# Kernel optimization log

Measured on AMD Instinct MI355X. Metric: run time of the kernel, lower is better.

## Reference

```python
import jax, jax.numpy as jnp
import numpy as np

B, N, E = 64, 2048, 32768          # graphs, nodes/graph, edges/graph
DIM = 64
RATIO = 0.8
K1 = int(np.ceil(RATIO * N))        # 1639 nodes/graph after pool1
K2 = int(np.ceil(RATIO * K1))       # 1312 nodes/graph after pool2
NUM_CLASSES = 6


def gcn_conv(x, W, b, src, dst, valid, n):
    # GCNConv with self-loops: out = D^-1/2 (A+I) D^-1/2 (x W) + b
    xw = x @ W                                          # [n, DIM]
    deg = jnp.zeros(n, x.dtype).at[dst].add(valid) + 1.0  # in-degree incl. self-loop
    norm = valid * jax.lax.rsqrt(deg[src] * deg[dst])      # per-edge norm (0 for masked)
    agg = jnp.zeros_like(xw).at[dst].add(xw[src] * norm[:, None])
    return agg + xw / deg[:, None] + b                  # self-loop term has norm 1/deg


def topk_pool(x, p, n_graphs, n_per, k):
    # PyG TopKPooling: score = tanh(x.p/||p||); keep top-k per graph; gate x by score
    score = jnp.tanh((x @ p) / jnp.linalg.norm(p))       # [n_graphs*n_per]
    vals, idx = jax.lax.top_k(score.reshape(n_graphs, n_per), k)  # [n_graphs, k]
    xg = x.reshape(n_graphs, n_per, -1)
    sel = jnp.take_along_axis(xg, idx[..., None], axis=1)          # [n_graphs, k, DIM]
    xp = sel * vals[..., None]
    perm = (idx + (jnp.arange(n_graphs) * n_per)[:, None]).reshape(-1)  # global ids kept
    return xp.reshape(n_graphs * k, -1), perm


def global_max_mean(x, n_graphs, n_per):
    xg = x.reshape(n_graphs, n_per, -1)
    return jnp.concatenate([xg.max(axis=1), xg.mean(axis=1)], axis=1)  # [n_graphs, 2*DIM]


def forward(x, edge_index, batch, W1, b1, p1, W2, b2, p2, lin1_w, lin1_b, lin2_w, lin2_b):
    src, dst = edge_index[0], edge_index[1]
    n_total = B * N
    ones = jnp.ones(src.shape[0], x.dtype)

    x = jax.nn.relu(gcn_conv(x, W1, b1, src, dst, ones, n_total))
    x, perm = topk_pool(x, p1, B, N, K1)
    x1 = global_max_mean(x, B, K1)

    # filter_adj: reindex edges to surviving nodes; drop (mask) edges touching removed nodes
    new_id = jnp.full(n_total, -1, jnp.int32).at[perm].set(jnp.arange(B * K1, dtype=jnp.int32))
    s2, d2 = new_id[src], new_id[dst]
    valid = ((s2 >= 0) & (d2 >= 0)).astype(x.dtype)
    s2 = jnp.where(s2 >= 0, s2, 0)
    d2 = jnp.where(d2 >= 0, d2, 0)

    x = jax.nn.relu(gcn_conv(x, W2, b2, s2, d2, valid, B * K1))
    x, _ = topk_pool(x, p2, B, K1, K2)
    x2 = global_max_mean(x, B, K2)

    h = x1 + x2
    h = jax.nn.relu(h @ lin1_w + lin1_b)
    return h @ lin2_w + lin2_b                           # [B, NUM_CLASSES]


def setup_inputs():
    key = jax.random.key(0)
    ks = jax.random.split(key, 10)
    x = jax.random.normal(ks[0], (B * N, DIM), jnp.float32)
    off = (jnp.arange(B) * N)[:, None]
    src = (jax.random.randint(ks[1], (B, E), 0, N) + off).reshape(-1)
    dst = (jax.random.randint(ks[2], (B, E), 0, N) + off).reshape(-1)
    edge_index = jnp.stack([src, dst]).astype(jnp.int32)
    batch = jnp.repeat(jnp.arange(B, dtype=jnp.int32), N)
    s = 1.0 / np.sqrt(DIM)
    return {
        "x": x,
        "edge_index": edge_index,
        "batch": batch,
        "W1": jax.random.normal(ks[3], (DIM, DIM), jnp.float32) * s,
        "b1": jnp.zeros(DIM, jnp.float32),
        "p1": jax.random.normal(ks[4], (DIM,), jnp.float32) * s,
        "W2": jax.random.normal(ks[5], (DIM, DIM), jnp.float32) * s,
        "b2": jnp.zeros(DIM, jnp.float32),
        "p2": jax.random.normal(ks[6], (DIM,), jnp.float32) * s,
        "lin1_w": jax.random.normal(ks[7], (2 * DIM, DIM), jnp.float32) / np.sqrt(2 * DIM),
        "lin1_b": jnp.zeros(DIM, jnp.float32),
        "lin2_w": jax.random.normal(ks[8], (DIM, NUM_CLASSES), jnp.float32) * s,
        "lin2_b": jnp.zeros(NUM_CLASSES, jnp.float32),
    }


def reference(x, edge_index, batch, W1, b1, p1, W2, b2, p2, lin1_w, lin1_b, lin2_w, lin2_b):
    return forward(x, edge_index, batch, W1, b1, p1, W2, b2, p2, lin1_w, lin1_b, lin2_w, lin2_b)
```

## Files before the change

### kernel.cpp

```cpp
#include <hip/hip_runtime.h>
#include <hip/hip_bf16.h>
#include <cstdint>
#include <cstddef>

#define B_    64
#define N_    2048
#define E_    32768
#define DIM_  64
#define K1_   1639
#define K2_   1312
#define NTOT  (B_ * N_)
#define ETOT  (B_ * E_)
#define N2TOT (B_ * K1_)
#define NCLS  6
#define PB_   8
#define CHUNKS_ 16
#define SLICES_ 16
#define BCAP  3072
#define REG_  192

typedef short bf8 __attribute__((ext_vector_type(8)));
typedef float f4  __attribute__((ext_vector_type(4)));

static __device__ __forceinline__ float2 bf2f(unsigned u) {
    float2 r;
    r.x = __uint_as_float(u << 16);
    r.y = __uint_as_float(u & 0xFFFF0000u);
    return r;
}
static __device__ __forceinline__ unsigned f2bf(float a, float b) {
    __hip_bfloat162 h = __float22bfloat162_rn(make_float2(a, b));
    unsigned u;
    __builtin_memcpy(&u, &h, 4);
    return u;
}
static __device__ __forceinline__ unsigned short f2bf_rn(float v) {
    unsigned u = __float_as_uint(v);
    return (unsigned short)((u + 0x7FFFu + ((u >> 16) & 1u)) >> 16);
}

template<int STAGE>
__launch_bounds__(256)
__global__ void k_bucket(const int* src, const int* dst, const int* remap,
                         int* bcnt, unsigned int* blist) {
    const int LSTR = (STAGE == 1) ? 128 : 103;
    __shared__ unsigned int lb[CHUNKS_][REG_];
    __shared__ int lc[CHUNKS_];
    int b = blockIdx.x;
    int g = b & 63, slice = b >> 6;
    int tid = threadIdx.x;
    if (tid < CHUNKS_) lc[tid] = 0;
    __syncthreads();
    const int ESL = E_ / SLICES_;
    const int* sp = src + (size_t)g * E_ + slice * ESL;
    const int* dp = dst + (size_t)g * E_ + slice * ESL;
    int gbase = g * ((STAGE == 1) ? N_ : K1_);
    for (int e = tid * 4; e < ESL; e += 1024) {
        int4 ss = *(const int4*)&sp[e];
        int4 dd = *(const int4*)&dp[e];
#pragma unroll
        for (int t = 0; t < 4; t++) {
            int s = (&ss.x)[t], d = (&dd.x)[t];
            if (STAGE == 2) {
                s = remap[s]; d = remap[d];
                if ((s | d) < 0) continue;
                s -= gbase; d -= gbase;
            } else {
                s &= (N_ - 1); d &= (N_ - 1);
            }
            int ch = d / LSTR;
            int dl = d - ch * LSTR;
            int p = atomicAdd(&lc[ch], 1);
            if (p < REG_) lb[ch][p] = ((unsigned)dl << 12) | (unsigned)s;
        }
    }
    __syncthreads();
    for (int ch = 0; ch < CHUNKS_; ch++) {
        int n = min(lc[ch], REG_);
        unsigned int* out = blist + (size_t)(g * CHUNKS_ + ch) * BCAP + slice * REG_;
        for (int i = tid; i < n; i += 256) out[i] = lb[ch][i];
    }
    if (tid < CHUNKS_) bcnt[(g * SLICES_ + slice) * CHUNKS_ + tid] = min(lc[tid], REG_);
}

template<int STAGE>
__launch_bounds__(256)
__global__ void k_sort(const int* bcnt, unsigned int* blist,
                       const float* xsrc, const int* sel, const float* vals,
                       unsigned int* xb, int* ninfo) {
    const int NL   = (STAGE == 1) ? N_ : K1_;
    const int LSTR = (STAGE == 1) ? 128 : 103;
    __shared__ int cnt[128], st[128], cur[128], cnt_s[SLICES_];
    __shared__ float rsqv[128];
    __shared__ unsigned short sorted[BCAP];
    int b = blockIdx.x;
    int g = b & 63, ch = b >> 6;
    int tid = threadIdx.x;
    if (tid < 128) { cnt[tid] = 0; cur[tid] = 0; }
    if (tid < SLICES_) cnt_s[tid] = bcnt[(g * SLICES_ + tid) * CHUNKS_ + ch];
    __syncthreads();
    size_t bb = (size_t)(g * CHUNKS_ + ch) * BCAP;
    const unsigned int* bl = blist + bb;
    for (int s = 0; s < SLICES_; s++) {
        int ns = cnt_s[s];
        for (int i = tid; i < ns; i += 256) atomicAdd(&cnt[bl[s * REG_ + i] >> 12], 1);
    }
    __syncthreads();
    if (tid < 128) st[tid] = cnt[tid];
    __syncthreads();
    for (int o = 1; o < 128; o <<= 1) {
        int add = (tid >= o && tid < 128) ? st[tid - o] : 0;
        __syncthreads();
        if (tid < 128) st[tid] += add;
        __syncthreads();
    }
    for (int s = 0; s < SLICES_; s++) {
        int ns = cnt_s[s];
        for (int i = tid; i < ns; i += 256) {
            unsigned pk = bl[s * REG_ + i];
            int dl = (int)(pk >> 12);
            int p = st[dl] - cnt[dl] + atomicAdd(&cur[dl], 1);
            sorted[p] = (unsigned short)(pk & 0xFFFu);
        }
    }
    __syncthreads();
    int n = st[127];
    for (int i = tid; i < n; i += 256) blist[bb + i] = (unsigned int)sorted[i];
    int lo = ch * LSTR;
    int nloc = min(LSTR, NL - lo);
    int gbase = g * NL;
    if (tid < nloc) {
        int node = gbase + lo + tid;
        int c = cnt[tid];
        int start = (int)bb + st[tid] - c;
        ninfo[node] = (start << 8) | min(c, 255);
        rsqv[tid] = rsqrtf((float)(c + 1));
    }
    __syncthreads();
    const float2* xs = (const float2*)xsrc;
    for (int idx = tid; idx < nloc * 32; idx += 256) {
        int nl = idx >> 5, f2 = idx & 31;
        int node = gbase + lo + nl;
        int rowp; float sc;
        if (STAGE == 2) { rowp = sel[node]; sc = vals[node] * rsqv[nl]; }
        else            { rowp = node;      sc = rsqv[nl]; }
        float2 v = xs[(size_t)rowp * 32 + f2];
        xb[(size_t)node * 32 + f2] = f2bf(v.x * sc, v.y * sc);
    }
}

template<bool GATE>
__launch_bounds__(256)
__global__ void k_agg(const unsigned int* xb, const int* ninfo, const unsigned int* csr,
                      float* y) {
    int b = blockIdx.x;
    int xcd = b & 7, r = b >> 3;
    int graph, local;
    if (GATE) {
        graph = xcd * 8 + r / 410;
        local = (r % 410) * 4 + (threadIdx.x >> 6);
        if (local >= K1_) return;
    } else {
        graph = xcd * 8 + (r >> 9);
        local = (r & 511) * 4 + (threadIdx.x >> 6);
    }
    const int NL = GATE ? K1_ : N_;
    int node = graph * NL + local;
    int lane = threadIdx.x & 63;
    int half = lane >> 5;
    int fpos = lane & 31;
    int ni = ninfo[node];
    int cnt = ni & 255, base = ni >> 8;
    float rd = rsqrtf((float)(cnt + 1));
    float ax = 0.f, ay = 0.f, bx = 0.f, by = 0.f;
    float cx = 0.f, cy = 0.f, dx = 0.f, dy = 0.f;
    int gbase = graph * NL;
    for (int chunk = 0; chunk < cnt; chunk += 64) {
        int nch = min(64, cnt - chunk);
        int sv = 0;
        if (lane < nch) sv = gbase + (int)csr[base + chunk + lane];
        int i = 0;
        for (; i + 8 <= nch; i += 8) {
            int s0 = __shfl(sv, i + half),     s1 = __shfl(sv, i + 2 + half),
                s2 = __shfl(sv, i + 4 + half), s3 = __shfl(sv, i + 6 + half);
            unsigned u0 = xb[(size_t)s0 * 32 + fpos];
            unsigned u1 = xb[(size_t)s1 * 32 + fpos];
            unsigned u2 = xb[(size_t)s2 * 32 + fpos];
            unsigned u3 = xb[(size_t)s3 * 32 + fpos];
            float2 f0 = bf2f(u0), f1 = bf2f(u1), f2 = bf2f(u2), f3 = bf2f(u3);
            ax += f0.x; ay += f0.y;
            bx += f1.x; by += f1.y;
            cx += f2.x; cy += f2.y;
            dx += f3.x; dy += f3.y;
        }
        for (; i + 4 <= nch; i += 4) {
            int s0 = __shfl(sv, i + half), s1 = __shfl(sv, i + 2 + half);
            unsigned u0 = xb[(size_t)s0 * 32 + fpos];
            unsigned u1 = xb[(size_t)s1 * 32 + fpos];
            float2 f0 = bf2f(u0), f1 = bf2f(u1);
            ax += f0.x; ay += f0.y;
            bx += f1.x; by += f1.y;
        }
        for (; i < nch; i += 2) {
            int idx = i + half;
            int s0 = __shfl(sv, idx & 63);
            float m = (idx < nch) ? 1.f : 0.f;
            float2 f0 = bf2f(xb[(size_t)s0 * 32 + fpos]);
            ax += f0.x * m; ay += f0.y * m;
        }
    }
    float sx = (ax + bx) + (cx + dx), sy = (ay + by) + (cy + dy);
    sx += __shfl(sx, lane ^ 32);
    sy += __shfl(sy, lane ^ 32);
    if (half == 0) {
        float2 fs = bf2f(xb[(size_t)node * 32 + fpos]);
        float2 o;
        o.x = (sx + fs.x) * rd;
        o.y = (sy + fs.y) * rd;
        ((float2*)y)[(size_t)node * 32 + fpos] = o;
    }
}

__launch_bounds__(256)
__global__ void k_convrow(float* y, const float* W, const float* bias, const float* pvec,
                          float* score, int rows) {
    int wid  = threadIdx.x >> 6;
    int lane = threadIdx.x & 63;
    int rowbase = blockIdx.x * 64 + wid * 16;
    int q = lane >> 4, c = lane & 15;
    bf8 bh[2][4], blo[2][4];
#pragma unroll
    for (int ks = 0; ks < 2; ks++)
#pragma unroll
        for (int nt = 0; nt < 4; nt++) {
            bf8 h, l;
#pragma unroll
            for (int j = 0; j < 8; j++) {
                float wv = W[(ks * 32 + q * 8 + j) * 64 + nt * 16 + c];
                unsigned short hb = f2bf_rn(wv);
                h[j] = (short)hb;
                l[j] = (short)f2bf_rn(wv - __uint_as_float((unsigned)hb << 16));
            }
            bh[ks][nt] = h; blo[ks][nt] = l;
        }
    const float* yr = y + (size_t)(rowbase + c) * DIM_ + q * 8;
    bf8 ah[2], al[2];
#pragma unroll
    for (int ks = 0; ks < 2; ks++) {
        float4 v0 = *(const float4*)(yr + ks * 32);
        float4 v1 = *(const float4*)(yr + ks * 32 + 4);
        float vv[8] = {v0.x, v0.y, v0.z, v0.w, v1.x, v1.y, v1.z, v1.w};
        bf8 h, l;
#pragma unroll
        for (int j = 0; j < 8; j++) {
            unsigned short hb = f2bf_rn(vv[j]);
            h[j] = (short)hb;
            l[j] = (short)f2bf_rn(vv[j] - __uint_as_float((unsigned)hb << 16));
        }
        ah[ks] = h; al[ks] = l;
    }
    float pp = 0.f;
#pragma unroll
    for (int i = 0; i < DIM_; i++) pp += pvec[i] * pvec[i];
    float rpn = rsqrtf(pp);
    float dot[4] = {0.f, 0.f, 0.f, 0.f};
#pragma unroll
    for (int nt = 0; nt < 4; nt++) {
        f4 acc = {0.f, 0.f, 0.f, 0.f};
#pragma unroll
        for (int ks = 0; ks < 2; ks++) {
            acc = __builtin_amdgcn_mfma_f32_16x16x32_bf16(ah[ks], bh[ks][nt],  acc, 0, 0, 0);
            acc = __builtin_amdgcn_mfma_f32_16x16x32_bf16(ah[ks], blo[ks][nt], acc, 0, 0, 0);
            acc = __builtin_amdgcn_mfma_f32_16x16x32_bf16(al[ks], bh[ks][nt],  acc, 0, 0, 0);
        }
        float bcol = bias[nt * 16 + c];
        float pcol = pvec[nt * 16 + c];
        float st[4];
#pragma unroll
        for (int reg = 0; reg < 4; reg++) {
            float v = fmaxf(acc[reg] + bcol, 0.f);
            st[reg] = v;
            dot[reg] += v * pcol;
        }
#pragma unroll
        for (int reg = 0; reg < 4; reg++)
            y[(size_t)(rowbase + q * 4 + reg) * DIM_ + nt * 16 + c] = st[reg];
    }
#pragma unroll
    for (int m = 1; m < 16; m <<= 1) {
#pragma unroll
        for (int reg = 0; reg < 4; reg++) dot[reg] += __shfl_xor(dot[reg], m);
    }
    if (c == 0) {
#pragma unroll
        for (int reg = 0; reg < 4; reg++)
            score[rowbase + q * 4 + reg] = tanhf(dot[reg] * rpn);
    }
    (void)rows;
}

template<int STAGE>
__launch_bounds__(256)
__global__ void k_select(const float* score, int* new_id, int* sel, float* vals) {
    const int Nin = (STAGE == 1) ? N_ : K1_;
    const int K   = (STAGE == 1) ? K1_ : K2_;
    __shared__ unsigned long long keys[N_];
    __shared__ int bins[256], ts[256];
    __shared__ unsigned long long s_prefix;
    __shared__ int s_need, s_cnt;
    int g = blockIdx.x, tid = threadIdx.x;
    const float* sg = score + (size_t)g * Nin;
    for (int i = tid; i < Nin; i += 256) {
        unsigned u = __float_as_uint(sg[i]);
        u = (u & 0x80000000u) ? ~u : (u | 0x80000000u);
        keys[i] = ((unsigned long long)u << 11) | (unsigned long long)(2047 - i);
    }
    if (tid == 0) { s_need = K; s_prefix = 0ull; s_cnt = 0; }
    __syncthreads();
    for (int shift = 40; shift >= 0; shift -= 8) {
        bins[tid] = 0;
        __syncthreads();
        unsigned long long pref = s_prefix;
        int need = s_need;
        int hi = shift + 8;
        for (int i = tid; i < Nin; i += 256) {
            unsigned long long k = keys[i];
            if ((k >> hi) == pref) atomicAdd(&bins[(int)((k >> shift) & 255)], 1);
        }
        __syncthreads();
        ts[tid] = bins[tid];
        __syncthreads();
        for (int o = 1; o < 256; o <<= 1) {
            int add = (tid + o < 256) ? ts[tid + o] : 0;
            __syncthreads();
            ts[tid] += add;
            __syncthreads();
        }
        int nxt = (tid == 255) ? 0 : ts[tid + 1];
        if (ts[tid] >= need && nxt < need) {
            s_prefix = (pref << 8) | (unsigned long long)tid;
            s_need = need - nxt;
        }
        __syncthreads();
    }
    unsigned long long T = s_prefix;
    for (int i = tid; i < Nin; i += 256) {
        if (keys[i] >= T) {
            int r = atomicAdd(&s_cnt, 1);
            int slot = g * K + r;
            sel[slot]  = g * Nin + i;
            vals[slot] = sg[i];
            if (STAGE == 1) new_id[g * N_ + i] = slot;
        } else if (STAGE == 1) {
            new_id[g * N_ + i] = -1;
        }
    }
}

template<int STAGE>
__launch_bounds__(256)
__global__ void k_pool(const float* conv, const int* sel, const float* vals, float* part) {
    const int K = (STAGE == 1) ? K1_ : K2_;
    int b = blockIdx.x;
    int g = b & 63, c = b >> 6;
    int wv = threadIdx.x >> 6, lane = threadIdx.x & 63;
    float mx = -3.402823466e38f, sm = 0.f;
    for (int r = c * 4 + wv; r < K; r += PB_ * 4) {
        int slot = g * K + r;
        int row  = sel[slot];
        float val = vals[slot];
        float v = conv[(size_t)row * DIM_ + lane] * val;
        mx = fmaxf(mx, v);
        sm += v;
    }
    __shared__ float rmx[4][64], rsm[4][64];
    rmx[wv][lane] = mx; rsm[wv][lane] = sm;
    __syncthreads();
    if (wv == 0) {
        mx = fmaxf(fmaxf(rmx[0][lane], rmx[1][lane]), fmaxf(rmx[2][lane], rmx[3][lane]));
        sm = rsm[0][lane] + rsm[1][lane] + rsm[2][lane] + rsm[3][lane];
        part[((size_t)(g * PB_ + c) * 2 + 0) * 64 + lane] = mx;
        part[((size_t)(g * PB_ + c) * 2 + 1) * 64 + lane] = sm;
    }
}

__launch_bounds__(64)
__global__ void k_head(const float* part1, const float* part2,
                       const float* l1w, const float* l1b,
                       const float* l2w, const float* l2b, float* out) {
    __shared__ float h[128];
    __shared__ float h1[64];
    int g = blockIdx.x, t = threadIdx.x;
    float mx1 = -3.402823466e38f, sm1 = 0.f, mx2 = -3.402823466e38f, sm2 = 0.f;
#pragma unroll
    for (int c = 0; c < PB_; c++) {
        mx1 = fmaxf(mx1, part1[((size_t)(g * PB_ + c) * 2 + 0) * 64 + t]);
        sm1 += part1[((size_t)(g * PB_ + c) * 2 + 1) * 64 + t];
        mx2 = fmaxf(mx2, part2[((size_t)(g * PB_ + c) * 2 + 0) * 64 + t]);
        sm2 += part2[((size_t)(g * PB_ + c) * 2 + 1) * 64 + t];
    }
    h[t]      = mx1 + mx2;
    h[t + 64] = sm1 / (float)K1_ + sm2 / (float)K2_;
    __syncthreads();
    float acc = l1b[t];
#pragma unroll 8
    for (int i = 0; i < 128; i++) acc += h[i] * l1w[i * 64 + t];
    h1[t] = fmaxf(acc, 0.0f);
    __syncthreads();
    if (t < NCLS) {
        float o = l2b[t];
#pragma unroll
        for (int i = 0; i < 64; i++) o += h1[i] * l2w[i * NCLS + t];
        out[g * NCLS + t] = o;
    }
}

extern "C" void kernel_launch(void* const* d_in, const int* in_sizes, int n_in,
                              void* d_out, int out_size, void* d_ws, size_t ws_size,
                              hipStream_t stream) {
    const float* x   = (const float*)d_in[0];
    const int*   ei  = (const int*)d_in[1];
    const int*   src = ei;
    const int*   dst = ei + ETOT;
    const float* W1  = (const float*)d_in[3];
    const float* b1  = (const float*)d_in[4];
    const float* p1  = (const float*)d_in[5];
    const float* W2  = (const float*)d_in[6];
    const float* b2  = (const float*)d_in[7];
    const float* p2  = (const float*)d_in[8];
    const float* l1w = (const float*)d_in[9];
    const float* l1b = (const float*)d_in[10];
    const float* l2w = (const float*)d_in[11];
    const float* l2b = (const float*)d_in[12];
    (void)in_sizes; (void)n_in; (void)out_size; (void)ws_size;

    char* ws = (char*)d_ws;
    size_t off = 0;
    auto alloc = [&](size_t bytes) -> void* {
        void* p = ws + off;
        off = (off + bytes + 255) & ~(size_t)255;
        return p;
    };
    float*        bufA  = (float*)       alloc((size_t)NTOT  * DIM_ * 4);
    float*        bufB  = (float*)       alloc((size_t)N2TOT * DIM_ * 4);
    unsigned int* blist = (unsigned int*)alloc((size_t)B_ * CHUNKS_ * BCAP * 4);
    unsigned int* xb    = (unsigned int*)alloc((size_t)NTOT * 32 * 4);
    int*          bcnt  = (int*)         alloc((size_t)B_ * SLICES_ * CHUNKS_ * 4);
    int*          ninfo = (int*)         alloc((size_t)NTOT * 4);
    float*        score = (float*)       alloc((size_t)NTOT * 4);
    int*          newid = (int*)         alloc((size_t)NTOT * 4);
    int*          sel1  = (int*)         alloc((size_t)N2TOT * 4);
    float*        vals1 = (float*)       alloc((size_t)N2TOT * 4);
    int*          sel2  = (int*)         alloc((size_t)B_ * K2_ * 4);
    float*        vals2 = (float*)       alloc((size_t)B_ * K2_ * 4);
    float*        part1 = (float*)       alloc((size_t)B_ * PB_ * 128 * 4);
    float*        part2 = (float*)       alloc((size_t)B_ * PB_ * 128 * 4);

    k_bucket<1><<<B_ * SLICES_, 256, 0, stream>>>(src, dst, nullptr, bcnt, blist);
    k_sort<1><<<B_ * CHUNKS_, 256, 0, stream>>>(bcnt, blist, x, nullptr, nullptr, xb, ninfo);
    k_agg<false><<<NTOT / 4, 256, 0, stream>>>(xb, ninfo, blist, bufA);
    k_convrow<<<NTOT / 64, 256, 0, stream>>>(bufA, W1, b1, p1, score, NTOT);
    k_select<1><<<B_, 256, 0, stream>>>(score, newid, sel1, vals1);
    k_pool<1><<<B_ * PB_, 256, 0, stream>>>(bufA, sel1, vals1, part1);

    k_bucket<2><<<B_ * SLICES_, 256, 0, stream>>>(src, dst, newid, bcnt, blist);
    k_sort<2><<<B_ * CHUNKS_, 256, 0, stream>>>(bcnt, blist, bufA, sel1, vals1, xb, ninfo);
    k_agg<true><<<410 * B_, 256, 0, stream>>>(xb, ninfo, blist, bufB);
    k_convrow<<<N2TOT / 64, 256, 0, stream>>>(bufB, W2, b2, p2, score, N2TOT);
    k_select<2><<<B_, 256, 0, stream>>>(score, nullptr, sel2, vals2);
    k_pool<2><<<B_ * PB_, 256, 0, stream>>>(bufB, sel2, vals2, part2);

    k_head<<<B_, 64, 0, stream>>>(part1, part2, l1w, l1b, l2w, l2b, (float*)d_out);
}
```

Baseline: 355.2 us.

## Stage remap in LDS, prescale CSR indices, wave-level scans, emit pooled bf16 features

Several independent tweaks. k_bucket stage 2 stages the per-graph remap table in shared memory instead of reading it from global memory for every edge. k_sort flattens its slice loops, replaces the block-wide Hillis-Steele scan with wave shuffle scans, and stores neighbour indices pre-multiplied by 32. k_agg uses those scaled indices to skip a multiply. k_select gets a shuffle-based suffix scan with fewer barriers. k_pool stage 1 also writes the gated pooled rows as bf16 into a compact buffer (aliased onto bufB), so stage-2 sort reads contiguous bf16 instead of gathering fp32 rows via sel and vals; this adds an extra bf16 rounding step.

```diff
diff --git a/kernel.cpp b/kernel.cpp
--- a/kernel.cpp
+++ b/kernel.cpp
@@ -46,10 +46,13 @@
     const int LSTR = (STAGE == 1) ? 128 : 103;
     __shared__ unsigned int lb[CHUNKS_][REG_];
     __shared__ int lc[CHUNKS_];
+    __shared__ int rm[N_];
     int b = blockIdx.x;
     int g = b & 63, slice = b >> 6;
     int tid = threadIdx.x;
     if (tid < CHUNKS_) lc[tid] = 0;
+    if (STAGE == 2)
+        for (int i = tid; i < N_; i += 256) rm[i] = remap[g * N_ + i];
     __syncthreads();
     const int ESL = E_ / SLICES_;
     const int* sp = src + (size_t)g * E_ + slice * ESL;
@@ -62,7 +65,7 @@
         for (int t = 0; t < 4; t++) {
             int s = (&ss.x)[t], d = (&dd.x)[t];
             if (STAGE == 2) {
-                s = remap[s]; d = remap[d];
+                s = rm[s & (N_ - 1)]; d = rm[d & (N_ - 1)];
                 if ((s | d) < 0) continue;
                 s -= gbase; d -= gbase;
             } else {
@@ -86,11 +89,11 @@
 template<int STAGE>
 __launch_bounds__(256)
 __global__ void k_sort(const int* bcnt, unsigned int* blist,
-                       const float* xsrc, const int* sel, const float* vals,
+                       const float* xf, const unsigned int* xg,
                        unsigned int* xb, int* ninfo) {
     const int NL   = (STAGE == 1) ? N_ : K1_;
     const int LSTR = (STAGE == 1) ? 128 : 103;
-    __shared__ int cnt[128], st[128], cur[128], cnt_s[SLICES_];
+    __shared__ int cnt[128], st[128], cur[128], cnt_s[SLICES_], stot[2];
     __shared__ float rsqv[128];
     __shared__ unsigned short sorted[BCAP];
     int b = blockIdx.x;
@@ -101,23 +104,30 @@
     __syncthreads();
     size_t bb = (size_t)(g * CHUNKS_ + ch) * BCAP;
     const unsigned int* bl = blist + bb;
-    for (int s = 0; s < SLICES_; s++) {
-        int ns = cnt_s[s];
-        for (int i = tid; i < ns; i += 256) atomicAdd(&cnt[bl[s * REG_ + i] >> 12], 1);
-    }
-    __syncthreads();
-    if (tid < 128) st[tid] = cnt[tid];
-    __syncthreads();
-    for (int o = 1; o < 128; o <<= 1) {
-        int add = (tid >= o && tid < 128) ? st[tid - o] : 0;
-        __syncthreads();
-        if (tid < 128) st[tid] += add;
-        __syncthreads();
-    }
-    for (int s = 0; s < SLICES_; s++) {
-        int ns = cnt_s[s];
-        for (int i = tid; i < ns; i += 256) {
-            unsigned pk = bl[s * REG_ + i];
+    const int TOT = SLICES_ * REG_;
+    for (int i = tid; i < TOT; i += 256) {
+        int s = i / REG_, j = i - s * REG_;
+        if (j < cnt_s[s]) atomicAdd(&cnt[bl[i] >> 12], 1);
+    }
+    __syncthreads();
+    if (tid < 128) {
+        int v = cnt[tid];
+        int l64 = tid & 63;
+#pragma unroll
+        for (int o = 1; o < 64; o <<= 1) {
+            int t = __shfl_up(v, o);
+            if (l64 >= o) v += t;
+        }
+        st[tid] = v;
+        if (l64 == 63) stot[tid >> 6] = v;
+    }
+    __syncthreads();
+    if (tid >= 64 && tid < 128) st[tid] += stot[0];
+    __syncthreads();
+    for (int i = tid; i < TOT; i += 256) {
+        int s = i / REG_, j = i - s * REG_;
+        if (j < cnt_s[s]) {
+            unsigned pk = bl[i];
             int dl = (int)(pk >> 12);
             int p = st[dl] - cnt[dl] + atomicAdd(&cur[dl], 1);
             sorted[p] = (unsigned short)(pk & 0xFFFu);
@@ -125,7 +135,7 @@
     }
     __syncthreads();
     int n = st[127];
-    for (int i = tid; i < n; i += 256) blist[bb + i] = (unsigned int)sorted[i];
+    for (int i = tid; i < n; i += 256) blist[bb + i] = ((unsigned int)sorted[i]) << 5;
     int lo = ch * LSTR;
     int nloc = min(LSTR, NL - lo);
     int gbase = g * NL;
@@ -137,14 +147,13 @@
         rsqv[tid] = rsqrtf((float)(c + 1));
     }
     __syncthreads();
-    const float2* xs = (const float2*)xsrc;
     for (int idx = tid; idx < nloc * 32; idx += 256) {
         int nl = idx >> 5, f2 = idx & 31;
         int node = gbase + lo + nl;
-        int rowp; float sc;
-        if (STAGE == 2) { rowp = sel[node]; sc = vals[node] * rsqv[nl]; }
-        else            { rowp = node;      sc = rsqv[nl]; }
-        float2 v = xs[(size_t)rowp * 32 + f2];
+        float sc = rsqv[nl];
+        float2 v;
+        if (STAGE == 1) v = ((const float2*)xf)[(size_t)node * 32 + f2];
+        else            v = bf2f(xg[(size_t)node * 32 + f2]);
         xb[(size_t)node * 32 + f2] = f2bf(v.x * sc, v.y * sc);
     }
 }
@@ -174,19 +183,19 @@
     float rd = rsqrtf((float)(cnt + 1));
     float ax = 0.f, ay = 0.f, bx = 0.f, by = 0.f;
     float cx = 0.f, cy = 0.f, dx = 0.f, dy = 0.f;
-    int gbase = graph * NL;
+    int gbase32 = graph * NL * 32;
     for (int chunk = 0; chunk < cnt; chunk += 64) {
         int nch = min(64, cnt - chunk);
         int sv = 0;
-        if (lane < nch) sv = gbase + (int)csr[base + chunk + lane];
+        if (lane < nch) sv = gbase32 + (int)csr[base + chunk + lane];
         int i = 0;
         for (; i + 8 <= nch; i += 8) {
             int s0 = __shfl(sv, i + half),     s1 = __shfl(sv, i + 2 + half),
                 s2 = __shfl(sv, i + 4 + half), s3 = __shfl(sv, i + 6 + half);
-            unsigned u0 = xb[(size_t)s0 * 32 + fpos];
-            unsigned u1 = xb[(size_t)s1 * 32 + fpos];
-            unsigned u2 = xb[(size_t)s2 * 32 + fpos];
-            unsigned u3 = xb[(size_t)s3 * 32 + fpos];
+            unsigned u0 = xb[(size_t)(s0 + fpos)];
+            unsigned u1 = xb[(size_t)(s1 + fpos)];
+            unsigned u2 = xb[(size_t)(s2 + fpos)];
+            unsigned u3 = xb[(size_t)(s3 + fpos)];
             float2 f0 = bf2f(u0), f1 = bf2f(u1), f2 = bf2f(u2), f3 = bf2f(u3);
             ax += f0.x; ay += f0.y;
             bx += f1.x; by += f1.y;
@@ -195,9 +204,8 @@
         }
         for (; i + 4 <= nch; i += 4) {
             int s0 = __shfl(sv, i + half), s1 = __shfl(sv, i + 2 + half);
-            unsigned u0 = xb[(size_t)s0 * 32 + fpos];
-            unsigned u1 = xb[(size_t)s1 * 32 + fpos];
-            float2 f0 = bf2f(u0), f1 = bf2f(u1);
+            float2 f0 = bf2f(xb[(size_t)(s0 + fpos)]);
+            float2 f1 = bf2f(xb[(size_t)(s1 + fpos)]);
             ax += f0.x; ay += f0.y;
             bx += f1.x; by += f1.y;
         }
@@ -205,7 +213,7 @@
             int idx = i + half;
             int s0 = __shfl(sv, idx & 63);
             float m = (idx < nch) ? 1.f : 0.f;
-            float2 f0 = bf2f(xb[(size_t)s0 * 32 + fpos]);
+            float2 f0 = bf2f(xb[(size_t)(s0 + fpos)]);
             ax += f0.x * m; ay += f0.y * m;
         }
     }
@@ -305,10 +313,11 @@
     const int Nin = (STAGE == 1) ? N_ : K1_;
     const int K   = (STAGE == 1) ? K1_ : K2_;
     __shared__ unsigned long long keys[N_];
-    __shared__ int bins[256], ts[256];
+    __shared__ int bins[256], wsum[4];
     __shared__ unsigned long long s_prefix;
     __shared__ int s_need, s_cnt;
     int g = blockIdx.x, tid = threadIdx.x;
+    int l64 = tid & 63, wid = tid >> 6;
     const float* sg = score + (size_t)g * Nin;
     for (int i = tid; i < Nin; i += 256) {
         unsigned u = __float_as_uint(sg[i]);
@@ -328,16 +337,18 @@
             if ((k >> hi) == pref) atomicAdd(&bins[(int)((k >> shift) & 255)], 1);
         }
         __syncthreads();
-        ts[tid] = bins[tid];
+        int mine = bins[tid];
+        int v = mine;
+#pragma unroll
+        for (int o = 1; o < 64; o <<= 1) {
+            int t = __shfl_down(v, o);
+            if (l64 + o < 64) v += t;
+        }
+        if (l64 == 0) wsum[wid] = v;
         __syncthreads();
-        for (int o = 1; o < 256; o <<= 1) {
-            int add = (tid + o < 256) ? ts[tid + o] : 0;
-            __syncthreads();
-            ts[tid] += add;
-            __syncthreads();
-        }
-        int nxt = (tid == 255) ? 0 : ts[tid + 1];
-        if (ts[tid] >= need && nxt < need) {
+        for (int w = wid + 1; w < 4; w++) v += wsum[w];
+        int nxt = v - mine;
+        if (v >= need && nxt < need) {
             s_prefix = (pref << 8) | (unsigned long long)tid;
             s_need = need - nxt;
         }
@@ -359,7 +370,8 @@
 
 template<int STAGE>
 __launch_bounds__(256)
-__global__ void k_pool(const float* conv, const int* sel, const float* vals, float* part) {
+__global__ void k_pool(const float* conv, const int* sel, const float* vals, float* part,
+                       unsigned int* xg) {
     const int K = (STAGE == 1) ? K1_ : K2_;
     int b = blockIdx.x;
     int g = b & 63, c = b >> 6;
@@ -372,6 +384,10 @@
         float v = conv[(size_t)row * DIM_ + lane] * val;
         mx = fmaxf(mx, v);
         sm += v;
+        if (STAGE == 1) {
+            unsigned pk = f2bf(v, __shfl_xor(v, 1));
+            if (!(lane & 1)) xg[(size_t)slot * 32 + (lane >> 1)] = pk;
+        }
     }
     __shared__ float rmx[4][64], rsm[4][64];
     rmx[wv][lane] = mx; rsm[wv][lane] = sm;
@@ -455,20 +471,21 @@
     float*        vals2 = (float*)       alloc((size_t)B_ * K2_ * 4);
     float*        part1 = (float*)       alloc((size_t)B_ * PB_ * 128 * 4);
     float*        part2 = (float*)       alloc((size_t)B_ * PB_ * 128 * 4);
+    unsigned int* xg    = (unsigned int*)bufB;
 
     k_bucket<1><<<B_ * SLICES_, 256, 0, stream>>>(src, dst, nullptr, bcnt, blist);
-    k_sort<1><<<B_ * CHUNKS_, 256, 0, stream>>>(bcnt, blist, x, nullptr, nullptr, xb, ninfo);
+    k_sort<1><<<B_ * CHUNKS_, 256, 0, stream>>>(bcnt, blist, x, nullptr, xb, ninfo);
     k_agg<false><<<NTOT / 4, 256, 0, stream>>>(xb, ninfo, blist, bufA);
     k_convrow<<<NTOT / 64, 256, 0, stream>>>(bufA, W1, b1, p1, score, NTOT);
     k_select<1><<<B_, 256, 0, stream>>>(score, newid, sel1, vals1);
-    k_pool<1><<<B_ * PB_, 256, 0, stream>>>(bufA, sel1, vals1, part1);
+    k_pool<1><<<B_ * PB_, 256, 0, stream>>>(bufA, sel1, vals1, part1, xg);
 
     k_bucket<2><<<B_ * SLICES_, 256, 0, stream>>>(src, dst, newid, bcnt, blist);
-    k_sort<2><<<B_ * CHUNKS_, 256, 0, stream>>>(bcnt, blist, bufA, sel1, vals1, xb, ninfo);
+    k_sort<2><<<B_ * CHUNKS_, 256, 0, stream>>>(bcnt, blist, nullptr, xg, xb, ninfo);
     k_agg<true><<<410 * B_, 256, 0, stream>>>(xb, ninfo, blist, bufB);
     k_convrow<<<N2TOT / 64, 256, 0, stream>>>(bufB, W2, b2, p2, score, N2TOT);
     k_select<2><<<B_, 256, 0, stream>>>(score, nullptr, sel2, vals2);
-    k_pool<2><<<B_ * PB_, 256, 0, stream>>>(bufB, sel2, vals2, part2);
+    k_pool<2><<<B_ * PB_, 256, 0, stream>>>(bufB, sel2, vals2, part2, nullptr);
 
     k_head<<<B_, 64, 0, stream>>>(part1, part2, l1w, l1b, l2w, l2b, (float*)d_out);
 }
```

Result: faster. 344.7 us (-3.0%).
